# Optimization experiments

Measured on AMD Instinct MI355X. Metric: run time of the kernel, lower is better.

The kernel has to match this reference:

```python
import jax, jax.numpy as jnp
import numpy as np

# Bernstein-basis theta coefficients for d=2 (calculate_theta2(2)),
# inv_coeff order: [x^0, x^1, x^2]
THETAS = ((3.0, -3.0, 0.75), (0.0, 3.0, -1.5), (0.0, 0.0, 0.75))
HIGH_ORDER = 2

N_NODES = 50000
N_EDGES = 800000
IN_DIM, HID_DIM, OUT_DIM = 128, 64, 2


def setup_inputs() -> dict:
    key = jax.random.key(0)
    ks = jax.random.split(key, 16)
    f32 = jnp.float32
    def w(k, shape, fan_in):
        return jax.random.normal(k, shape, dtype=f32) * (1.0 / np.sqrt(fan_in))
    return {
        "in_feat": jax.random.normal(ks[0], (N_NODES, IN_DIM), dtype=f32),
        "src": jax.random.randint(ks[1], (N_EDGES,), 0, N_NODES, dtype=jnp.int32),
        "dst": jax.random.randint(ks[2], (N_EDGES,), 0, N_NODES, dtype=jnp.int32),
        "W1": w(ks[3], (IN_DIM, HID_DIM), IN_DIM), "b1": jnp.zeros((HID_DIM,), f32),
        "W2": w(ks[4], (HID_DIM, HID_DIM), HID_DIM), "b2": jnp.zeros((HID_DIM,), f32),
        "W3": w(ks[5], (HID_DIM * 5, HID_DIM), HID_DIM * 5), "b3": jnp.zeros((HID_DIM,), f32),
        "W4": w(ks[6], (HID_DIM, OUT_DIM), HID_DIM), "b4": jnp.zeros((OUT_DIM,), f32),
        "Wg1": w(ks[7], (IN_DIM, HID_DIM), IN_DIM), "bg1": jnp.zeros((HID_DIM,), f32),
        "Wg2": w(ks[8], (HID_DIM, IN_DIM), HID_DIM), "bg2": jnp.zeros((IN_DIM,), f32),
    }


def _spmm(x, src, dst, n):
    # y[v] = sum_{(u,v) in E} x[u]   (DGL update_all(copy_u, sum))
    return jax.ops.segment_sum(x[src], dst, num_segments=n)


def reference(in_feat, src, dst, W1, b1, W2, b2, W3, b3, W4, b4, Wg1, bg1, Wg2, bg2):
    n = in_feat.shape[0]
    ones_e = jnp.ones(src.shape[0], dtype=in_feat.dtype)
    deg_in = jnp.clip(jax.ops.segment_sum(ones_e, dst, num_segments=n), 1.0)
    deg_out = jnp.clip(jax.ops.segment_sum(ones_e, src, num_segments=n), 1.0)
    din = (deg_in ** -0.5)[:, None]   # [N,1]
    dout = (deg_out ** -0.5)[:, None]

    def lap(f):
        # f - D^{-1/2} A D^{-1/2} f  (in-degree norm, as in unnLaplacian)
        return f - _spmm(f * din, src, dst, n) * din

    # MLP front-end
    h = jax.nn.relu(in_feat @ W1 + b1)
    h = jax.nn.relu(h @ W2 + b2)

    branches = []
    # BandConv branches (lin=False): theta-weighted Laplacian polynomial
    for theta in THETAS:
        f = h
        acc = theta[0] * h
        for k in range(1, len(theta)):
            f = lap(f)
            acc = acc + theta[k] * f
        branches.append(acc)
    # HighConv branches: repeated Laplacian, num_layer = 1..HIGH_ORDER
    f = h
    for j in range(HIGH_ORDER):
        f = lap(f)
        branches.append(f)

    h_final = jnp.concatenate(branches, axis=-1)  # [N, 5*hid]
    out = jax.nn.relu(h_final @ W3 + b3) @ W4 + b4  # [N, out_dim]

    # GCN branch on self-loop-free graph (same edges here): symmetric norm GraphConv
    def gconv(x, W, b):
        return _spmm(x * dout, src, dst, n) * din @ W + b
    emb = gconv(jax.nn.relu(gconv(in_feat, Wg1, bg1)), Wg2, bg2)  # [N, in_dim]

    return out, emb
```

## Files before the change

kernel.cpp:

```cpp
#include <hip/hip_runtime.h>
#include <hip/hip_bf16.h>
#include <math.h>

#define NN 50000
#define NE 800000
#define C64 64
#define CE 12500
#define RW 12500
#define NW 25000
#define HISTB 128
#define RB 98
#define GB 782
#define ZSB 782
#define FSB 25000

typedef _Float16 half8 __attribute__((ext_vector_type(8)));
typedef _Float16 half4v __attribute__((ext_vector_type(4)));
typedef float f32x4 __attribute__((ext_vector_type(4)));

static inline int cdiv(int a, int b) { return (a + b - 1) / b; }


__device__ inline size_t pack_pos(int k, int n, int K, int M) {
    int tile = n >> 4;
    int kstep = k >> 5;
    int quad = (k >> 3) & 3;
    int j = k & 7;
    int lane = (quad << 4) | (n & 15);
    return ((size_t)(tile * (K >> 5) + kstep) * 64 + lane) * 8 + j;
}

__device__ void pack_std_dev(int bx, const float* __restrict__ W, _Float16* __restrict__ Wpk,
                             int K, int M) {
    int idx = bx * 256 + threadIdx.x;
    if (idx >= K * M) return;
    int k = idx / M, n = idx % M;
    Wpk[pack_pos(k, n, K, M)] = (_Float16)W[idx];
}

__device__ void pack_wc_dev(int bx, const float* __restrict__ W3, _Float16* __restrict__ wcpk) {
    int idx = bx * 256 + threadIdx.x;
    if (idx >= 3 * 4096) return;
    int b = idx >> 12;
    int rem = idx & 4095;
    int k = rem >> 6, n = rem & 63;
    float w0 = W3[(0 * 64 + k) * 64 + n];
    float w1 = W3[(1 * 64 + k) * 64 + n];
    float w2 = W3[(2 * 64 + k) * 64 + n];
    float w3 = W3[(3 * 64 + k) * 64 + n];
    float w4 = W3[(4 * 64 + k) * 64 + n];
    float v;
    if (b == 0)      v = 3.f * w0;
    else if (b == 1) v = -3.f * w0 + 3.f * w1 + w3;
    else             v = 0.75f * w0 - 1.5f * w1 + 0.75f * w2 + w4;
    wcpk[pack_pos(b * 64 + k, n, 192, 64)] = (_Float16)v;
}

__launch_bounds__(256)
__global__ void k_init(const float* __restrict__ W1, _Float16* __restrict__ W1pk,
                       const float* __restrict__ W2, _Float16* __restrict__ W2pk,
                       const float* __restrict__ Wg1, _Float16* __restrict__ Wg1pk,
                       const float* __restrict__ Wg2, _Float16* __restrict__ Wg2pk,
                       const float* __restrict__ W3, _Float16* __restrict__ wcpk) {
    int bx = blockIdx.x;
    if (bx < 32) { pack_std_dev(bx, W1, W1pk, 128, 64); return; }
    bx -= 32;
    if (bx < 16) { pack_std_dev(bx, W2, W2pk, 64, 64); return; }
    bx -= 16;
    if (bx < 32) { pack_std_dev(bx, Wg1, Wg1pk, 128, 64); return; }
    bx -= 32;
    if (bx < 32) { pack_std_dev(bx, Wg2, Wg2pk, 64, 128); return; }
    bx -= 32;
    pack_wc_dev(bx, W3, wcpk);
}


__device__ void hist_dev(int bx, const int* __restrict__ idx, unsigned* __restrict__ H,
                         unsigned* __restrict__ cnt) {
    int c = bx & 63, r = bx >> 6;
    int tid = threadIdx.x;
    for (int j = tid; j < RW; j += 256) cnt[j] = 0;
    __syncthreads();
    int lo = r * 25000;
    const int* p = idx + c * CE;
    for (int i = tid; i < CE; i += 256) {
        int v = p[i] - lo;
        if ((unsigned)v < 25000u)
            atomicAdd(&cnt[v >> 1], 1u << ((v & 1) * 16));
    }
    __syncthreads();
    unsigned* outp = H + (size_t)c * NW + r * RW;
    for (int j = tid; j < RW; j += 256) outp[j] = cnt[j];
}

__device__ void reduce_dev(int bx, const unsigned* __restrict__ H, int* __restrict__ dgo,
                           float* __restrict__ o_rsq, float* __restrict__ o_inv,
                           float* __restrict__ o_sq) {
    int w = bx * 256 + threadIdx.x;
    if (w >= NW) return;
    unsigned slo = 0, shi = 0;
#pragma unroll 8
    for (int c = 0; c < 64; c++) {
        unsigned h = H[(size_t)c * NW + w];
        slo += h & 0xffffu; shi += h >> 16;
    }
    if (dgo) {
        dgo[2 * w]     = slo > 64u ? 64 : (int)slo;
        dgo[2 * w + 1] = shi > 64u ? 64 : (int)shi;
    }
    float f0 = (float)(slo < 1u ? 1u : slo);
    float f1 = (float)(shi < 1u ? 1u : shi);
    o_rsq[2 * w] = rsqrtf(f0); o_rsq[2 * w + 1] = rsqrtf(f1);
    if (o_inv) { o_inv[2 * w] = 1.f / f0; o_inv[2 * w + 1] = 1.f / f1; }
    if (o_sq)  { o_sq[2 * w] = sqrtf(f0); o_sq[2 * w + 1] = sqrtf(f1); }
}

__device__ void prefix_dev(int bx, const unsigned* __restrict__ HD, unsigned* __restrict__ baseD) {
    int w = bx * 256 + threadIdx.x;
    if (w >= NW) return;
    unsigned slo = 0, shi = 0;
    for (int c = 0; c < 64; c++) {
        unsigned b0 = slo > 64u ? 64u : slo;
        unsigned b1 = shi > 64u ? 64u : shi;
        baseD[(size_t)c * NW + w] = b0 | (b1 << 16);
        unsigned h = HD[(size_t)c * NW + w];
        slo += h & 0xffffu; shi += h >> 16;
    }
}

__device__ void scatter_dev(int bx, const int* __restrict__ src, const int* __restrict__ dst,
                            const unsigned* __restrict__ baseD,
                            unsigned short* __restrict__ colsPad,
                            unsigned* __restrict__ cnt) {
    int c = bx & 63, r = bx >> 6;
    int tid = threadIdx.x;
    for (int j = tid; j < RW; j += 256) cnt[j] = 0;
    __syncthreads();
    int lo = r * 25000;
    const int* pd = dst + c * CE;
    const int* ps = src + c * CE;
    for (int i = tid; i < CE; i += 256) {
        int v = pd[i];
        int lv = v - lo;
        if ((unsigned)lv < 25000u) {
            unsigned old = atomicAdd(&cnt[lv >> 1], 1u << ((lv & 1) * 16));
            unsigned rank = (old >> ((lv & 1) * 16)) & 0xffffu;
            unsigned base = (baseD[(size_t)c * NW + (v >> 1)] >> ((v & 1) * 16)) & 0xffffu;
            unsigned pos = base + rank;
            if (pos < 64u) colsPad[(size_t)v * 64 + pos] = (unsigned short)ps[i];
        }
    }
}

__device__ void zscale_dev(int bx, half8* __restrict__ zh8, const float* __restrict__ dout, int N) {
    int idx = bx * 256 + threadIdx.x;
    if (idx >= N * 4) return;
    int row = idx >> 2;
    float m = dout[row];
    half8 a = zh8[idx * 2], b = zh8[idx * 2 + 1];
#pragma unroll
    for (int j = 0; j < 8; j++) {
        a[j] = (_Float16)((float)a[j] * m);
        b[j] = (_Float16)((float)b[j] * m);
    }
    zh8[idx * 2] = a; zh8[idx * 2 + 1] = b;
}


struct HSegs { const _Float16* p[3]; int ld[3]; };

template <int M, int K, bool OUTW, bool RSCA>
__device__ void mg_dev(int bx, HSegs A, const half8* __restrict__ Wpk,
                       const float* __restrict__ bias, int relu,
                       float* __restrict__ C,
                       _Float16* __restrict__ Ch0, const float* __restrict__ ms0,
                       const float* __restrict__ rsc,
                       const float* __restrict__ W4, const float* __restrict__ b4,
                       float* __restrict__ outp, int N) {
    constexpr int NT = M / 16;
    constexpr int NKS = K / 32;
    int tid = threadIdx.x;
    int wave = tid >> 6, lane = tid & 63;
    int quad = lane >> 4, m = lane & 15;
    int row0 = bx * 64 + wave * 16;
    int rowA = row0 + m; if (rowA >= N) rowA = N - 1;
    _Float16 hs = (_Float16)1.f;
    if (RSCA) hs = (_Float16)rsc[rowA];
    f32x4 acc[NT];
#pragma unroll
    for (int t = 0; t < NT; t++) acc[t] = (f32x4){0.f, 0.f, 0.f, 0.f};
#pragma unroll
    for (int ks = 0; ks < NKS; ks++) {
        const _Float16* ap = A.p[ks >> 1] + (size_t)rowA * A.ld[ks >> 1] + (ks & 1) * 32 + quad * 8;
        half8 af = *(const half8*)ap;
        if (RSCA) {
#pragma unroll
            for (int j = 0; j < 8; j++) af[j] *= hs;
        }
#pragma unroll
        for (int t = 0; t < NT; t++) {
            half8 bf = Wpk[(t * NKS + ks) * 64 + lane];
            acc[t] = __builtin_amdgcn_mfma_f32_16x16x32_f16(af, bf, acc[t], 0, 0, 0);
        }
    }
    float outv[NT][4];
#pragma unroll
    for (int t = 0; t < NT; t++) {
        float bv = bias ? bias[t * 16 + m] : 0.f;
#pragma unroll
        for (int r = 0; r < 4; r++) {
            float v = acc[t][r] + bv;
            if (relu) v = fmaxf(v, 0.f);
            outv[t][r] = v;
        }
    }
    if (OUTW) {
        float w40[NT], w41[NT];
#pragma unroll
        for (int t = 0; t < NT; t++) {
            w40[t] = W4[(t * 16 + m) * 2];
            w41[t] = W4[(t * 16 + m) * 2 + 1];
        }
#pragma unroll
        for (int r = 0; r < 4; r++) {
            float p0 = 0.f, p1 = 0.f;
#pragma unroll
            for (int t = 0; t < NT; t++) {
                p0 += outv[t][r] * w40[t];
                p1 += outv[t][r] * w41[t];
            }
#pragma unroll
            for (int off = 1; off < 16; off <<= 1) {
                p0 += __shfl_xor(p0, off);
                p1 += __shfl_xor(p1, off);
            }
            int row = row0 + quad * 4 + r;
            if (m == 0 && row < N) {
                outp[(size_t)row * 2 + 0] = p0 + b4[0];
                outp[(size_t)row * 2 + 1] = p1 + b4[1];
            }
        }
    }
    if (C || Ch0) {
#pragma unroll
        for (int r = 0; r < 4; r++) {
            int row = row0 + quad * 4 + r;
            if (row >= N) continue;
            float m0 = (Ch0 && ms0) ? ms0[row] : 1.f;
#pragma unroll
            for (int t = 0; t < NT; t++) {
                size_t off = (size_t)row * M + t * 16 + m;
                if (C)   C[off] = outv[t][r];
                if (Ch0) Ch0[off] = (_Float16)(outv[t][r] * m0);
            }
        }
    }
}

__device__ void a15_dev(int bx, const float* __restrict__ in_feat,
                        const half8* __restrict__ W1pk, const half8* __restrict__ Wg1pk,
                        const float* __restrict__ b1,
                        _Float16* __restrict__ h1h, _Float16* __restrict__ zh, int N) {
    int tid = threadIdx.x;
    int wave = tid >> 6, lane = tid & 63;
    int quad = lane >> 4, m = lane & 15;
    int row0 = bx * 64 + wave * 16;
    int rowA = row0 + m; if (rowA >= N) rowA = N - 1;
    f32x4 acc0[4], acc1[4];
#pragma unroll
    for (int t = 0; t < 4; t++) {
        acc0[t] = (f32x4){0.f, 0.f, 0.f, 0.f};
        acc1[t] = (f32x4){0.f, 0.f, 0.f, 0.f};
    }
#pragma unroll
    for (int ks = 0; ks < 4; ks++) {
        const float* ap = in_feat + (size_t)rowA * 128 + ks * 32 + quad * 8;
        float4 u = *(const float4*)ap;
        float4 v = *(const float4*)(ap + 4);
        half8 af;
        af[0] = (_Float16)u.x; af[1] = (_Float16)u.y; af[2] = (_Float16)u.z; af[3] = (_Float16)u.w;
        af[4] = (_Float16)v.x; af[5] = (_Float16)v.y; af[6] = (_Float16)v.z; af[7] = (_Float16)v.w;
#pragma unroll
        for (int t = 0; t < 4; t++) {
            acc0[t] = __builtin_amdgcn_mfma_f32_16x16x32_f16(af, W1pk[(t * 4 + ks) * 64 + lane], acc0[t], 0, 0, 0);
            acc1[t] = __builtin_amdgcn_mfma_f32_16x16x32_f16(af, Wg1pk[(t * 4 + ks) * 64 + lane], acc1[t], 0, 0, 0);
        }
    }
#pragma unroll
    for (int r = 0; r < 4; r++) {
        int row = row0 + quad * 4 + r;
        if (row >= N) continue;
#pragma unroll
        for (int t = 0; t < 4; t++) {
            float v0 = fmaxf(acc0[t][r] + b1[t * 16 + m], 0.f);
            h1h[(size_t)row * 64 + t * 16 + m] = (_Float16)v0;
            zh[(size_t)row * 64 + t * 16 + m] = (_Float16)acc1[t][r];
        }
    }
}


__launch_bounds__(256)
__global__ void k_L1(const int* __restrict__ src, const int* __restrict__ dst,
                     unsigned* __restrict__ HD, unsigned* __restrict__ HS,
                     const float* __restrict__ in_feat,
                     const half8* __restrict__ W1pk, const half8* __restrict__ Wg1pk,
                     const float* __restrict__ b1,
                     _Float16* __restrict__ h1h, _Float16* __restrict__ zh, int N) {
    __shared__ unsigned cnt[RW];
    int bx = blockIdx.x;
    if (bx < HISTB) { hist_dev(bx, dst, HD, cnt); return; }
    bx -= HISTB;
    if (bx < HISTB) { hist_dev(bx, src, HS, cnt); return; }
    bx -= HISTB;
    a15_dev(bx, in_feat, W1pk, Wg1pk, b1, h1h, zh, N);
}

__launch_bounds__(256)
__global__ void k_L2(const unsigned* __restrict__ HD, const unsigned* __restrict__ HS,
                     int* __restrict__ degin, float* __restrict__ din,
                     float* __restrict__ din2, float* __restrict__ dsq,
                     float* __restrict__ dout, unsigned* __restrict__ baseD) {
    int bx = blockIdx.x;
    if (bx < RB) { reduce_dev(bx, HD, degin, din, din2, dsq); return; }
    bx -= RB;
    if (bx < RB) { reduce_dev(bx, HS, nullptr, dout, nullptr, nullptr); return; }
    bx -= RB;
    prefix_dev(bx, HD, baseD);
}

__launch_bounds__(256)
__global__ void k_L3(const int* __restrict__ src, const int* __restrict__ dst,
                     const unsigned* __restrict__ baseD, unsigned short* __restrict__ colsPad,
                     const _Float16* __restrict__ h1h, const half8* __restrict__ W2pk,
                     const float* __restrict__ b2, _Float16* __restrict__ u0h,
                     const float* __restrict__ din,
                     half8* __restrict__ zh8, const float* __restrict__ dout, int N) {
    __shared__ unsigned cnt[RW];
    int bx = blockIdx.x;
    if (bx < HISTB) { scatter_dev(bx, src, dst, baseD, colsPad, cnt); return; }
    bx -= HISTB;
    if (bx < GB) {
        HSegs A;
        A.p[0] = h1h; A.ld[0] = 64;
        A.p[1] = nullptr; A.ld[1] = 0;
        A.p[2] = nullptr; A.ld[2] = 0;
        mg_dev<64, 64, false, false>(bx, A, W2pk, b2, 1, nullptr, u0h, din,
                                     nullptr, nullptr, nullptr, nullptr, N);
        return;
    }
    bx -= GB;
    zscale_dev(bx, zh8, dout, N);
}


struct SpmmP {
    const half4v* xh; const half4v* fsub_h; const float* rowscale; const float* bias;
    half4v* yh0; const float* ms0; int relu;
};

__launch_bounds__(256)
__global__ void k_FS(SpmmP P0, SpmmP P1, const unsigned short* __restrict__ colsPad,
                     const int* __restrict__ deg, int N) {
    int bx = blockIdx.x;
    int g = bx >> 3, x = bx & 7;
    bool first = x < 4;
    SpmmP P = first ? P0 : P1;
    int row = g * 16 + (x & 3) * 4 + (threadIdx.x >> 6);
    if (row >= N) return;
    int lane = threadIdx.x & 63;
    int sub = lane >> 4, c = lane & 15;
    int dg = deg[row];
    int base = row * 64;
    int e = base + sub;
    int end = base + dg;
    float ax = 0.f, ay = 0.f, az = 0.f, aw = 0.f;
    for (; e + 12 < end; e += 16) {
        int s0 = colsPad[e], s1 = colsPad[e + 4], s2 = colsPad[e + 8], s3 = colsPad[e + 12];
        half4v v0 = P.xh[(size_t)s0 * 16 + c];
        half4v v1 = P.xh[(size_t)s1 * 16 + c];
        half4v v2 = P.xh[(size_t)s2 * 16 + c];
        half4v v3 = P.xh[(size_t)s3 * 16 + c];
        ax += (float)v0.x + (float)v1.x + (float)v2.x + (float)v3.x;
        ay += (float)v0.y + (float)v1.y + (float)v2.y + (float)v3.y;
        az += (float)v0.z + (float)v1.z + (float)v2.z + (float)v3.z;
        aw += (float)v0.w + (float)v1.w + (float)v2.w + (float)v3.w;
    }
    for (; e < end; e += 4) {
        int s = colsPad[e];
        half4v v = P.xh[(size_t)s * 16 + c];
        ax += (float)v.x; ay += (float)v.y; az += (float)v.z; aw += (float)v.w;
    }
    ax += __shfl_xor(ax, 16); ay += __shfl_xor(ay, 16);
    az += __shfl_xor(az, 16); aw += __shfl_xor(aw, 16);
    ax += __shfl_xor(ax, 32); ay += __shfl_xor(ay, 32);
    az += __shfl_xor(az, 32); aw += __shfl_xor(aw, 32);
    if (sub != 0) return;
    size_t oidx = (size_t)row * 16 + c;
    if (P.fsub_h) {
        float d = P.rowscale[row];
        half4v f = P.fsub_h[oidx];
        ax = (float)f.x - ax * d; ay = (float)f.y - ay * d;
        az = (float)f.z - az * d; aw = (float)f.w - aw * d;
    } else {
        if (P.rowscale) { float d = P.rowscale[row]; ax *= d; ay *= d; az *= d; aw *= d; }
        if (P.bias) {
            float4 bb = ((const float4*)P.bias)[c];
            ax += bb.x; ay += bb.y; az += bb.z; aw += bb.w;
        }
        if (P.relu) {
            ax = fmaxf(ax, 0.f); ay = fmaxf(ay, 0.f);
            az = fmaxf(az, 0.f); aw = fmaxf(aw, 0.f);
        }
    }
    float mm = P.ms0 ? P.ms0[row] : 1.f;
    half4v h;
    h.x = (_Float16)(ax * mm); h.y = (_Float16)(ay * mm);
    h.z = (_Float16)(az * mm); h.w = (_Float16)(aw * mm);
    P.yh0[oidx] = h;
}

__launch_bounds__(256)
__global__ void k_F3(const _Float16* __restrict__ u0h, const _Float16* __restrict__ u1h,
                     const _Float16* __restrict__ u2h, const half8* __restrict__ wcpk,
                     const float* __restrict__ b3, const float* __restrict__ dsq,
                     const float* __restrict__ W4, const float* __restrict__ b4,
                     float* __restrict__ outp,
                     const _Float16* __restrict__ sgh, const half8* __restrict__ Wg2pk,
                     const float* __restrict__ bg2, float* __restrict__ emb, int N) {
    int bx = blockIdx.x;
    if (bx < GB) {
        HSegs A;
        A.p[0] = u0h; A.ld[0] = 64;
        A.p[1] = u1h; A.ld[1] = 64;
        A.p[2] = u2h; A.ld[2] = 64;
        mg_dev<64, 192, true, true>(bx, A, wcpk, b3, 1, nullptr, nullptr, nullptr,
                                    dsq, W4, b4, outp, N);
        return;
    }
    bx -= GB;
    HSegs A;
    A.p[0] = sgh; A.ld[0] = 64;
    A.p[1] = nullptr; A.ld[1] = 0;
    A.p[2] = nullptr; A.ld[2] = 0;
    mg_dev<128, 64, false, false>(bx, A, Wg2pk, bg2, 0, emb, nullptr, nullptr,
                                  nullptr, nullptr, nullptr, nullptr, N);
}

extern "C" void kernel_launch(void* const* d_in, const int* in_sizes, int n_in,
                              void* d_out, int out_size, void* d_ws, size_t ws_size,
                              hipStream_t stream) {
    const int N = NN;
    const float* in_feat = (const float*)d_in[0];
    const int* src = (const int*)d_in[1];
    const int* dst = (const int*)d_in[2];
    const float* W1 = (const float*)d_in[3];
    const float* b1 = (const float*)d_in[4];
    const float* W2 = (const float*)d_in[5];
    const float* b2 = (const float*)d_in[6];
    const float* W3 = (const float*)d_in[7];
    const float* b3 = (const float*)d_in[8];
    const float* W4 = (const float*)d_in[9];
    const float* b4 = (const float*)d_in[10];
    const float* Wg1 = (const float*)d_in[11];
    const float* bg1 = (const float*)d_in[12];
    const float* Wg2 = (const float*)d_in[13];
    const float* bg2 = (const float*)d_in[14];

    float* out = (float*)d_out;
    float* emb = out + (size_t)N * 2;

    float* fw = (float*)d_ws;
    float* din  = fw;
    float* din2 = din + N;
    float* dsq  = din2 + N;
    float* dout = dsq + N;
    int* degin  = (int*)(dout + N);
    unsigned short* colsPad = (unsigned short*)(degin + N);
    unsigned* HD   = (unsigned*)(colsPad + (size_t)64 * N);
    unsigned* HS   = HD + (size_t)C64 * NW;
    unsigned* baseD = HS + (size_t)C64 * NW;
    _Float16* hp = (_Float16*)(baseD + (size_t)C64 * NW);
    _Float16* h1h   = hp;
    _Float16* u0h   = h1h + (size_t)64 * N;
    _Float16* u1h   = u0h + (size_t)64 * N;
    _Float16* u2h   = u1h + (size_t)64 * N;
    _Float16* zh    = u2h + (size_t)64 * N;
    _Float16* g1h   = zh + (size_t)64 * N;
    _Float16* sgh   = g1h + (size_t)64 * N;
    _Float16* W1pk  = sgh + (size_t)64 * N;
    _Float16* W2pk  = W1pk + 8192;
    _Float16* Wg1pk = W2pk + 4096;
    _Float16* Wg2pk = Wg1pk + 8192;
    _Float16* wcpk  = Wg2pk + 8192;

    k_init<<<160, 256, 0, stream>>>(W1, W1pk, W2, W2pk, Wg1, Wg1pk, Wg2, Wg2pk, W3, wcpk);

    k_L1<<<2 * HISTB + GB, 256, 0, stream>>>(src, dst, HD, HS, in_feat,
        (const half8*)W1pk, (const half8*)Wg1pk, b1, h1h, zh, N);

    k_L2<<<2 * RB + RB, 256, 0, stream>>>(HD, HS, degin, din, din2, dsq, dout, baseD);

    k_L3<<<HISTB + GB + ZSB, 256, 0, stream>>>(src, dst, baseD, colsPad,
        h1h, (const half8*)W2pk, b2, u0h, din, (half8*)zh, dout, N);

    SpmmP p0, p1;
    p0 = {(const half4v*)u0h, (const half4v*)u0h, din2, nullptr, (half4v*)u1h, nullptr, 0};
    p1 = {(const half4v*)zh, nullptr, din, bg1, (half4v*)g1h, dout, 1};
    k_FS<<<FSB, 256, 0, stream>>>(p0, p1, colsPad, degin, N);

    p0 = {(const half4v*)u1h, (const half4v*)u1h, din2, nullptr, (half4v*)u2h, nullptr, 0};
    p1 = {(const half4v*)g1h, nullptr, nullptr, nullptr, (half4v*)sgh, din, 0};
    k_FS<<<FSB, 256, 0, stream>>>(p0, p1, colsPad, degin, N);

    k_F3<<<2 * GB, 256, 0, stream>>>(u0h, u1h, u2h, (const half8*)wcpk, b3, dsq,
        W4, b4, out, sgh, (const half8*)Wg2pk, bg2, emb, N);
}
```

Baseline: 290.1 us.

## Map one row per 16-lane quad in SpMM gather kernel, drop shuffle reduction

The gather SpMM kernel previously gave each row a full 64-lane wave split into four edge sub-streams, then merged them with cross-lane shuffles. Now each 16-lane quad owns one row and walks all of its edges serially, loading four column indices at once as a vector. The grid is cut to a quarter of the blocks, with the two problem instances split into contiguous block ranges. This removes the shuffle reduction and the idle lanes on low-degree rows, but lengthens each lane's serial dependency chain and reduces memory-level parallelism per row.

```diff
diff --git a/kernel.cpp b/kernel.cpp
--- a/kernel.cpp
+++ b/kernel.cpp
@@ -12,7 +12,8 @@
 #define RB 98
 #define GB 782
 #define ZSB 782
-#define FSB 25000
+#define FSG 3125
+#define FSB 6250
 
 typedef _Float16 half8 __attribute__((ext_vector_type(8)));
 typedef _Float16 half4v __attribute__((ext_vector_type(4)));
@@ -359,43 +360,40 @@
     half4v* yh0; const float* ms0; int relu;
 };
 
+typedef unsigned short ushort4v __attribute__((ext_vector_type(4)));
+
 __launch_bounds__(256)
 __global__ void k_FS(SpmmP P0, SpmmP P1, const unsigned short* __restrict__ colsPad,
                      const int* __restrict__ deg, int N) {
     int bx = blockIdx.x;
-    int g = bx >> 3, x = bx & 7;
-    bool first = x < 4;
+    bool first = bx < FSG;
     SpmmP P = first ? P0 : P1;
-    int row = g * 16 + (x & 3) * 4 + (threadIdx.x >> 6);
+    int g = first ? bx : bx - FSG;
+    int tid = threadIdx.x;
+    int wave = tid >> 6, lane = tid & 63;
+    int quad = lane >> 4, c = lane & 15;
+    int row = g * 16 + wave * 4 + quad;
     if (row >= N) return;
-    int lane = threadIdx.x & 63;
-    int sub = lane >> 4, c = lane & 15;
     int dg = deg[row];
-    int base = row * 64;
-    int e = base + sub;
-    int end = base + dg;
+    const unsigned short* cp = colsPad + (size_t)row * 64;
     float ax = 0.f, ay = 0.f, az = 0.f, aw = 0.f;
-    for (; e + 12 < end; e += 16) {
-        int s0 = colsPad[e], s1 = colsPad[e + 4], s2 = colsPad[e + 8], s3 = colsPad[e + 12];
-        half4v v0 = P.xh[(size_t)s0 * 16 + c];
-        half4v v1 = P.xh[(size_t)s1 * 16 + c];
-        half4v v2 = P.xh[(size_t)s2 * 16 + c];
-        half4v v3 = P.xh[(size_t)s3 * 16 + c];
+    int e = 0;
+    for (; e + 3 < dg; e += 4) {
+        ushort4v ss = *(const ushort4v*)(cp + e);
+        half4v v0 = P.xh[(size_t)ss.x * 16 + c];
+        half4v v1 = P.xh[(size_t)ss.y * 16 + c];
+        half4v v2 = P.xh[(size_t)ss.z * 16 + c];
+        half4v v3 = P.xh[(size_t)ss.w * 16 + c];
         ax += (float)v0.x + (float)v1.x + (float)v2.x + (float)v3.x;
         ay += (float)v0.y + (float)v1.y + (float)v2.y + (float)v3.y;
         az += (float)v0.z + (float)v1.z + (float)v2.z + (float)v3.z;
         aw += (float)v0.w + (float)v1.w + (float)v2.w + (float)v3.w;
     }
-    for (; e < end; e += 4) {
-        int s = colsPad[e];
+    for (; e < dg; e++) {
+        int s = cp[e];
         half4v v = P.xh[(size_t)s * 16 + c];
         ax += (float)v.x; ay += (float)v.y; az += (float)v.z; aw += (float)v.w;
     }
-    ax += __shfl_xor(ax, 16); ay += __shfl_xor(ay, 16);
-    az += __shfl_xor(az, 16); aw += __shfl_xor(aw, 16);
-    ax += __shfl_xor(ax, 32); ay += __shfl_xor(ay, 32);
-    az += __shfl_xor(az, 32); aw += __shfl_xor(aw, 32);
-    if (sub != 0) return;
     size_t oidx = (size_t)row * 16 + c;
     if (P.fsub_h) {
         float d = P.rowscale[row];
```

After: 266.2 us. -8.2%, faster.
